# Kernel optimization log

Measured on AMD Instinct MI355X. Metric: run time of the kernel, lower is better.

The kernel has to match this reference:

```python
import jax, jax.numpy as jnp
import numpy as np

B, C, H, W = 8, 256, 48, 48
QC = C // 8                # query/key channels
MIP = max(8, C // 32)      # CoordAtt bottleneck channels
EPS = 1e-5                 # BatchNorm eps (inference, running_mean=0, running_var=1)


def _conv1x1(x, Wt, b=None):
    # 1x1 conv == channel matmul: x [b,c,h,w], Wt [o,c]
    y = jnp.einsum('bchw,oc->bohw', x, Wt)
    if b is not None:
        y = y + b[None, :, None, None]
    return y


def _bn(x, w, b):
    # inference BatchNorm with running_mean=0, running_var=1
    s = w * np.float32(1.0 / np.sqrt(1.0 + EPS))
    return x * s[None, :, None, None] + b[None, :, None, None]


def setup_inputs() -> dict:
    key = jax.random.key(0)
    ks = jax.random.split(key, 22)
    r = lambda k, sh, s=0.05: jax.random.normal(k, sh, jnp.float32) * s
    return dict(
        f1=jax.random.normal(ks[0], (B, C, H, W), jnp.float32),
        f2=jax.random.normal(ks[1], (B, C, H, W), jnp.float32),
        t1=r(ks[2], (1, C, 1, 1), 1.0),
        t2=r(ks[3], (1, C, 1, 1), 1.0),
        Wq=r(ks[4], (QC, C)), bq=r(ks[5], (QC,)),
        Wk=r(ks[6], (QC, C)), bk=r(ks[7], (QC,)),
        Wv=r(ks[8], (C, C)), bv=r(ks[9], (C,)),
        gamma=jnp.full((1,), 0.5, jnp.float32),
        ca_w1=r(ks[10], (MIP, C)), ca_b1=r(ks[11], (MIP,)),
        ca_bn_w=1.0 + r(ks[12], (MIP,)), ca_bn_b=r(ks[13], (MIP,)),
        ca_wh=r(ks[14], (C, MIP)), ca_bh=r(ks[15], (C,)),
        ca_ww=r(ks[16], (C, MIP)), ca_bw=r(ks[17], (C,)),
        fus_w=r(ks[18], (C, 2 * C)),
        fus_bn_w=1.0 + r(ks[19], (C,)), fus_bn_b=r(ks[20], (C,)),
    )


def _cross_attention(f1, f2, t1, t2, Wq, bq, Wk, bk, Wv, bv, gamma):
    b, c, h, w = f1.shape
    N = h * w
    f1e = f1 + t1
    f2e = f2 + t2

    def qkv(fe):
        q = _conv1x1(fe, Wq, bq).reshape(b, QC, N).transpose(0, 2, 1)  # [b,N,qc]
        k = _conv1x1(fe, Wk, bk).reshape(b, QC, N)                     # [b,qc,N]
        v = _conv1x1(fe, Wv, bv).reshape(b, c, N)                      # [b,c,N]
        return q, k, v

    q1, k1, v1 = qkv(f1e)
    q2, k2, v2 = qkv(f2e)

    # CrossAtt_1 = softmax(Q2 @ K1^T) applied to V1
    attn21 = jax.nn.softmax(jnp.einsum('bmq,bqn->bmn', q2, k1), axis=-1)  # [b,N,N]
    out1 = jnp.einsum('bcn,bmn->bcm', v1, attn21).reshape(b, c, h, w)
    # CrossAtt_2 = softmax(Q1 @ K2^T) applied to V2
    attn12 = jax.nn.softmax(jnp.einsum('bmq,bqn->bmn', q1, k2), axis=-1)
    out2 = jnp.einsum('bcn,bmn->bcm', v2, attn12).reshape(b, c, h, w)

    return gamma[0] * out1 + f1, gamma[0] * out2 + f2


def _coord_att(x, w1, b1, bnw, bnb, wh, bh, ww, bw):
    b, c, h, w = x.shape
    x_h = jnp.mean(x, axis=3, keepdims=True)                         # [b,c,h,1]
    x_w = jnp.mean(x, axis=2, keepdims=True).transpose(0, 1, 3, 2)   # [b,c,w,1]
    y = jnp.concatenate([x_h, x_w], axis=2)                          # [b,c,h+w,1]
    y = jax.nn.relu(_bn(_conv1x1(y, w1, b1), bnw, bnb))
    yh, yw = y[:, :, :h], y[:, :, h:]
    a_h = jax.nn.sigmoid(_conv1x1(yh, wh, bh))                       # [b,c,h,1]
    a_w = jax.nn.sigmoid(_conv1x1(yw.transpose(0, 1, 3, 2), ww, bw)) # [b,c,1,w]
    return x * a_w * a_h


def _fusion(x, Wf, bnw, bnb):
    return jax.nn.relu(_bn(_conv1x1(x, Wf), bnw, bnb))


def reference(f1, f2, t1, t2, Wq, bq, Wk, bk, Wv, bv, gamma,
              ca_w1, ca_b1, ca_bn_w, ca_bn_b, ca_wh, ca_bh, ca_ww, ca_bw,
              fus_w, fus_bn_w, fus_bn_b):
    a1, a2 = _cross_attention(f1, f2, t1, t2, Wq, bq, Wk, bk, Wv, bv, gamma)
    c1 = _coord_att(f1, ca_w1, ca_b1, ca_bn_w, ca_bn_b, ca_wh, ca_bh, ca_ww, ca_bw)
    c2 = _coord_att(f2, ca_w1, ca_b1, ca_bn_w, ca_bn_b, ca_wh, ca_bh, ca_ww, ca_bw)
    o1 = _fusion(jnp.concatenate([a1, c1], axis=1), fus_w, fus_bn_w, fus_bn_b)
    o2 = _fusion(jnp.concatenate([a2, c2], axis=1), fus_w, fus_bn_w, fus_bn_b)
    return o1, o2
```

## Files before the change

kernel.cpp:

```cpp
#include <hip/hip_runtime.h>
#include <hip/hip_bf16.h>

typedef unsigned short ushort_t;
typedef __attribute__((ext_vector_type(8))) short short8;
typedef __attribute__((ext_vector_type(4))) float floatx4;
typedef __attribute__((ext_vector_type(16))) float floatx16;
typedef __attribute__((ext_vector_type(4))) unsigned int uintx4;


__device__ __forceinline__ float bf2f(ushort_t u) {
    return __uint_as_float(((unsigned int)u) << 16);
}
__device__ __forceinline__ ushort_t f2bf(float f) {
    unsigned int x = __float_as_uint(f);
    unsigned int r = (x + 0x7fffu + ((x >> 16) & 1u)) >> 16;
    return (ushort_t)r;
}
__device__ __forceinline__ unsigned int pkbf(float a, float b) {
    __hip_bfloat162 h = __float22bfloat162_rn(float2{a, b});
    return *reinterpret_cast<unsigned int*>(&h);
}
__device__ __forceinline__ float loadIn(const void* p, size_t i, int isbf) {
    return isbf ? bf2f(((const ushort_t*)p)[i]) : ((const float*)p)[i];
}
__device__ __forceinline__ float fexp2(float x) {
#if __has_builtin(__builtin_amdgcn_exp2f)
    return __builtin_amdgcn_exp2f(x);
#else
    return exp2f(x);
#endif
}
__device__ __forceinline__ void plswap(unsigned& a, unsigned& b, int h) {
#if __has_builtin(__builtin_amdgcn_permlane32_swap)
    auto r = __builtin_amdgcn_permlane32_swap(a, b, false, false);
    a = r[0];
    b = r[1];
#else
    unsigned sa = __shfl_xor(a, 32), sb = __shfl_xor(b, 32);
    unsigned na = (h == 0) ? a : sb;
    unsigned nb = (h == 0) ? sa : b;
    a = na; b = nb;
#endif
}

#define BN_SCALE 0.9999950000374997f
#define LOG2E    1.4426950408889634f
#define ZERO16 (floatx16){0.f,0.f,0.f,0.f,0.f,0.f,0.f,0.f,0.f,0.f,0.f,0.f,0.f,0.f,0.f,0.f}

#define P_T1    0
#define P_T2    256
#define P_WQ    512
#define P_BQ    8704
#define P_WK    8768
#define P_BK    16960
#define P_WV    17024
#define P_BV    82560
#define P_GAMMA 82624
#define P_CAW1  82688
#define P_CAB1  84736
#define P_BNW   84800
#define P_BNB   84864
#define P_WH    84928
#define P_BH    86976
#define P_WW    87232
#define P_BW    89280
#define P_FUSW  89536
#define P_FBNW  220608
#define P_FBNB  220864
#define P_BQ2   221120

#define ATTN_BLOCKS 1152

__global__ void detect_kernel(const void* gamma, int* flag) {
    if (threadIdx.x == 0) {
        ushort_t u = ((const ushort_t*)gamma)[0];
        *flag = (u != 0) ? 1 : 0;
    }
}

__global__ __launch_bounds__(256) void convert_params(
    const void* t1, const void* t2, const void* Wq, const void* bq,
    const void* Wk, const void* bk, const void* Wv, const void* bv,
    const void* gm, const void* cw1, const void* cb1, const void* bnw,
    const void* bnb, const void* wh, const void* bh, const void* ww,
    const void* bw, const void* fw, const void* fbnw, const void* fbnb,
    const int* flagp, float* dst, ushort_t* WA, ushort_t* WF)
{
    int isbf = *flagp;
    const void* srcs[20] = {t1,t2,Wq,bq,Wk,bk,Wv,bv,gm,cw1,cb1,bnw,bnb,wh,bh,ww,bw,fw,fbnw,fbnb};
    const int   cnts[20] = {256,256,8192,32,8192,32,65536,256,1,2048,8,8,8,2048,256,2048,256,131072,256,256};
    const int   offs[20] = {P_T1,P_T2,P_WQ,P_BQ,P_WK,P_BK,P_WV,P_BV,P_GAMMA,P_CAW1,P_CAB1,
                            P_BNW,P_BNB,P_WH,P_BH,P_WW,P_BW,P_FUSW,P_FBNW,P_FBNB};
    int tid = blockIdx.x * 256 + threadIdx.x;
    int stride = gridDim.x * 256;
    #pragma unroll
    for (int sg = 0; sg < 20; sg++) {
        float* d = dst + offs[sg];
        for (int i = tid; i < cnts[sg]; i += stride) d[i] = loadIn(srcs[sg], i, isbf);
    }
    for (int i = tid; i < 81920; i += stride) {
        int o = i >> 8, c = i & 255;
        float v;
        if (o < 32)      v = loadIn(Wq, o * 256 + c, isbf);
        else if (o < 64) v = loadIn(Wk, (o - 32) * 256 + c, isbf);
        else             v = loadIn(Wv, (size_t)(o - 64) * 256 + c, isbf);
        WA[i] = f2bf(v);
    }
    for (int i = tid; i < 131072; i += stride) WF[i] = f2bf(loadIn(fw, i, isbf));
    int gw = tid >> 6, lane = tid & 63;
    if (gw < 640) {
        int side = gw / 320, o = gw % 320;
        const void* tsrc = side ? t2 : t1;
        float bias; const void* Wsrc; size_t wbase;
        if (o < 32)      { bias = loadIn(bq, o, isbf);       Wsrc = Wq; wbase = (size_t)o * 256; }
        else if (o < 64) { bias = loadIn(bk, o - 32, isbf);  Wsrc = Wk; wbase = (size_t)(o - 32) * 256; }
        else             { bias = loadIn(bv, o - 64, isbf);  Wsrc = Wv; wbase = (size_t)(o - 64) * 256; }
        float s = 0.f;
        for (int c = lane; c < 256; c += 64) s += loadIn(Wsrc, wbase + c, isbf) * loadIn(tsrc, c, isbf);
        s += __shfl_xor(s, 1);  s += __shfl_xor(s, 2);  s += __shfl_xor(s, 4);
        s += __shfl_xor(s, 8);  s += __shfl_xor(s, 16); s += __shfl_xor(s, 32);
        if (lane == 0) dst[P_BQ2 + gw] = bias + s;
    }
}

__global__ __launch_bounds__(256) void prep_qkv(
    const void* __restrict__ f1, const void* __restrict__ f2,
    const int* __restrict__ flagp,
    const ushort_t* __restrict__ WA, const float* __restrict__ P,
    ushort_t* __restrict__ fT,
    ushort_t* __restrict__ qG, ushort_t* __restrict__ kG, ushort_t* __restrict__ vG)
{
    __shared__ ushort_t xs[64][264];
    int isbf = *flagp;
    int blk = blockIdx.x;
    int nt = blk % 36, sb = blk / 36;
    int side = sb >> 3, b = sb & 7;
    int n0 = nt * 64;
    const void* f = side ? f2 : f1;
    int t = threadIdx.x;
    size_t base = ((size_t)b * 256 + t) * 2304 + n0;
    if (isbf) {
        const ushort_t* fp = (const ushort_t*)f + base;
        #pragma unroll
        for (int i = 0; i < 8; i++) {
            uint4 raw = *(const uint4*)&fp[i * 8];
            const ushort_t* rp = (const ushort_t*)&raw;
            #pragma unroll
            for (int j = 0; j < 8; j++) xs[i * 8 + j][t] = rp[j];
        }
    } else {
        const float* fp = (const float*)f + base;
        #pragma unroll
        for (int i = 0; i < 16; i++) {
            float4 raw = *(const float4*)&fp[i * 4];
            unsigned u0 = pkbf(raw.x, raw.y), u1 = pkbf(raw.z, raw.w);
            xs[i * 4 + 0][t] = (ushort_t)u0;
            xs[i * 4 + 1][t] = (ushort_t)(u0 >> 16);
            xs[i * 4 + 2][t] = (ushort_t)u1;
            xs[i * 4 + 3][t] = (ushort_t)(u1 >> 16);
        }
    }
    __syncthreads();
    #pragma unroll
    for (int i = 0; i < 8; i++) {
        int chunk = i * 256 + t;
        int row = chunk >> 5, k8 = (chunk & 31) * 8;
        *(uint4*)&fT[((size_t)sb * 2304 + n0 + row) * 256 + k8] = *(const uint4*)&xs[row][k8];
    }
    int w = t >> 6, l = t & 63, q = l >> 4, ln = l & 15;
    floatx4 acc[5][4];
    #pragma unroll
    for (int mi = 0; mi < 5; mi++)
        #pragma unroll
        for (int ns = 0; ns < 4; ns++) acc[mi][ns] = (floatx4){0.f, 0.f, 0.f, 0.f};
    #pragma unroll
    for (int ks = 0; ks < 8; ks++) {
        short8 a[5];
        #pragma unroll
        for (int mi = 0; mi < 5; mi++)
            a[mi] = *(const short8*)&WA[(size_t)(w * 80 + mi * 16 + ln) * 256 + ks * 32 + q * 8];
        #pragma unroll
        for (int ns = 0; ns < 4; ns++) {
            short8 bfr = *(const short8*)&xs[ns * 16 + ln][ks * 32 + q * 8];
            #pragma unroll
            for (int mi = 0; mi < 5; mi++)
                acc[mi][ns] = __builtin_amdgcn_mfma_f32_16x16x32_bf16(a[mi], bfr, acc[mi][ns], 0, 0, 0);
        }
    }
    const float* bp = P + P_BQ2 + side * 320;
    #pragma unroll
    for (int mi = 0; mi < 5; mi++) {
        int o0 = w * 80 + mi * 16 + q * 4;
        #pragma unroll
        for (int ns = 0; ns < 4; ns++) {
            int n = n0 + ns * 16 + ln;
            if (o0 < 32) {
                uint2 pk;
                pk.x = pkbf((acc[mi][ns][0] + bp[o0]) * LOG2E, (acc[mi][ns][1] + bp[o0 + 1]) * LOG2E);
                pk.y = pkbf((acc[mi][ns][2] + bp[o0 + 2]) * LOG2E, (acc[mi][ns][3] + bp[o0 + 3]) * LOG2E);
                *(uint2*)&qG[((size_t)sb * 2304 + n) * 32 + o0] = pk;
            } else if (o0 < 64) {
                uint2 pk;
                pk.x = pkbf(acc[mi][ns][0] + bp[o0], acc[mi][ns][1] + bp[o0 + 1]);
                pk.y = pkbf(acc[mi][ns][2] + bp[o0 + 2], acc[mi][ns][3] + bp[o0 + 3]);
                *(uint2*)&kG[((size_t)sb * 2304 + n) * 32 + (o0 - 32)] = pk;
            } else {
                unsigned u0 = pkbf(acc[mi][ns][0] + bp[o0], acc[mi][ns][1] + bp[o0 + 1]);
                unsigned u1 = pkbf(acc[mi][ns][2] + bp[o0 + 2], acc[mi][ns][3] + bp[o0 + 3]);
                vG[((size_t)sb * 256 + (o0 - 64 + 0)) * 2304 + n] = (ushort_t)u0;
                vG[((size_t)sb * 256 + (o0 - 64 + 1)) * 2304 + n] = (ushort_t)(u0 >> 16);
                vG[((size_t)sb * 256 + (o0 - 64 + 2)) * 2304 + n] = (ushort_t)u1;
                vG[((size_t)sb * 256 + (o0 - 64 + 3)) * 2304 + n] = (ushort_t)(u1 >> 16);
            }
        }
    }
}

__global__ __launch_bounds__(256) void pool_kernel(
    const ushort_t* __restrict__ fT, float* __restrict__ pools,
    float* __restrict__ lsum)
{
    int blk = blockIdx.x;
    int c = threadIdx.x;
    if (blk < 576 && c < 64) lsum[blk * 64 + c] = 0.f;
    int j = blk % 96, sb = blk / 96;
    const ushort_t* base = fT + (size_t)sb * 2304 * 256 + c;
    float s = 0.f;
    if (j < 48) {
        int h = j;
        #pragma unroll 8
        for (int w = 0; w < 48; w++) s += bf2f(base[(size_t)(h * 48 + w) * 256]);
    } else {
        int w = j - 48;
        #pragma unroll 8
        for (int h = 0; h < 48; h++) s += bf2f(base[(size_t)(h * 48 + w) * 256]);
    }
    pools[(size_t)sb * 24576 + c * 96 + j] = s * (1.f / 48.f);
}

__global__ __launch_bounds__(256) void attn_coord(
    const ushort_t* __restrict__ qG, const ushort_t* __restrict__ kG,
    const ushort_t* __restrict__ vG,
    ushort_t* __restrict__ O0, ushort_t* __restrict__ O1,
    float* __restrict__ lsum,
    const float* __restrict__ pools, const float* __restrict__ P,
    float* __restrict__ attv)
{
    __shared__ __align__(16) ushort_t vsm[4][64 * 68];
    __shared__ __align__(16) ushort_t paf[8192];

    int t = threadIdx.x;

    if (blockIdx.x >= ATTN_BLOCKS) {
        float* w1s = (float*)&vsm[0][0];
        float* ys  = w1s + 2048;
        int sb = blockIdx.x - ATTN_BLOCKS;
        for (int ff = t; ff < 2048; ff += 256) w1s[ff] = P[P_CAW1 + ff];
        __syncthreads();
        const float* pin = pools + (size_t)sb * 24576;
        if (t < 96) {
            float s[8];
            #pragma unroll
            for (int mp = 0; mp < 8; mp++) s[mp] = 0.f;
            for (int c = 0; c < 256; c++) {
                float p = pin[c * 96 + t];
                #pragma unroll
                for (int mp = 0; mp < 8; mp++) s[mp] += w1s[mp * 256 + c] * p;
            }
            #pragma unroll
            for (int mp = 0; mp < 8; mp++) {
                float vv = s[mp] + P[P_CAB1 + mp];
                vv = vv * (P[P_BNW + mp] * BN_SCALE) + P[P_BNB + mp];
                ys[mp * 96 + t] = fmaxf(vv, 0.f);
            }
        }
        __syncthreads();
        float* aout = attv + (size_t)sb * 24576;
        for (int ff = t; ff < 24576; ff += 256) {
            int j = ff >> 8, c = ff & 255;
            const float* W = P + ((j < 48) ? P_WH : P_WW);
            const float* B = P + ((j < 48) ? P_BH : P_BW);
            float s = B[c];
            #pragma unroll
            for (int mp = 0; mp < 8; mp++) s += W[c * 8 + mp] * ys[mp * 96 + j];
            aout[ff] = 1.f / (1.f + __expf(-s));
        }
        return;
    }

    int i = blockIdx.x;
    int xcd = i & 7, slot = i >> 3;
    int dhi = (slot >= 72) ? 1 : 0;
    int db = xcd + (dhi << 3);
    int rem = slot - 72 * dhi;
    int sp = rem & 1, mt = rem >> 1;
    int qsb = db ^ 8;

    int w = t >> 6;
    int qsw = w & 1, ksw = w >> 1;
    int l = t & 63, r31 = l & 31, h = l >> 5;
    int q0 = mt * 64, c0 = w * 64;

    short8 qf0, qf1;
    {
        const ushort_t* qrow = qG + ((size_t)qsb * 2304 + q0 + qsw * 32 + r31) * 32;
        qf0 = *(const short8*)&qrow[h * 8];
        qf1 = *(const short8*)&qrow[16 + h * 8];
    }

    const ushort_t* kW = kG + ((size_t)db * 2304 + ksw * 32 + r31) * 32 + h * 8;
    const ushort_t* vbase = vG + ((size_t)db * 256 + c0) * 2304;
    ushort_t* vw = &vsm[w][0];
    int vls = (l >> 3);
    int vlc = (l & 7) * 8;

    floatx16 o[2][2];
    #pragma unroll
    for (int qs = 0; qs < 2; qs++)
        #pragma unroll
        for (int cs = 0; cs < 2; cs++) o[qs][cs] = ZERO16;
    float l_lane = 0.f;

    int nstart = sp * 1152;

#define V_LOAD(VR, N0)                                                         \
    _Pragma("unroll")                                                          \
    for (int i_ = 0; i_ < 8; i_++) {                                           \
        int r_ = i_ * 8 + vls;                                                 \
        VR[i_] = *(const uint4*)&vbase[(size_t)r_ * 2304 + (N0) + vlc];        \
    }
#define V_STORE(VR)                                                            \
    _Pragma("unroll")                                                          \
    for (int i_ = 0; i_ < 8; i_++) {                                           \
        int a_ = (i_ * 8 + vls) * 68 + vlc;                                    \
        *(uint2*)&vw[a_]     = make_uint2(VR[i_].x, VR[i_].y);                 \
        *(uint2*)&vw[a_ + 4] = make_uint2(VR[i_].z, VR[i_].w);                 \
    }

#define DO_S_PUBLISH(K0, K1, BUF)                                              \
    {                                                                          \
        floatx16 s_ = ZERO16;                                                  \
        s_ = __builtin_amdgcn_mfma_f32_32x32x16_bf16(K0, qf0, s_, 0, 0, 0);    \
        s_ = __builtin_amdgcn_mfma_f32_32x32x16_bf16(K1, qf1, s_, 0, 0, 0);    \
        float e_[16];                                                          \
        _Pragma("unroll")                                                      \
        for (int r_ = 0; r_ < 16; r_++) e_[r_] = fexp2(s_[r_]);                \
        l_lane += (((e_[0] + e_[1]) + (e_[2] + e_[3]))                         \
                 + ((e_[4] + e_[5]) + (e_[6] + e_[7])))                        \
                + (((e_[8] + e_[9]) + (e_[10] + e_[11]))                       \
                 + ((e_[12] + e_[13]) + (e_[14] + e_[15])));                   \
        unsigned wd_[8];                                                       \
        _Pragma("unroll")                                                      \
        for (int p_ = 0; p_ < 8; p_++) wd_[p_] = pkbf(e_[2 * p_], e_[2 * p_ + 1]); \
        plswap(wd_[0], wd_[2], h); plswap(wd_[1], wd_[3], h);                  \
        plswap(wd_[4], wd_[6], h); plswap(wd_[5], wd_[7], h);                  \
        uintx4 A0_ = {wd_[0], wd_[1], wd_[2], wd_[3]};                         \
        uintx4 A1_ = {wd_[4], wd_[5], wd_[6], wd_[7]};                         \
        *(uintx4*)&paf[(size_t)((((BUF) * 2 + qsw) * 4 + ksw * 2 + 0) * 64 + l) * 8] = A0_; \
        *(uintx4*)&paf[(size_t)((((BUF) * 2 + qsw) * 4 + ksw * 2 + 1) * 64 + l) * 8] = A1_; \
    }

#define DO_PV(BUF)                                                             \
    __builtin_amdgcn_s_setprio(1);                                             \
    _Pragma("unroll")                                                          \
    for (int kt = 0; kt < 4; kt++) {                                           \
        short8 af0 = *(const short8*)&paf[(size_t)((((BUF) * 2 + 0) * 4 + kt) * 64 + l) * 8]; \
        short8 af1 = *(const short8*)&paf[(size_t)((((BUF) * 2 + 1) * 4 + kt) * 64 + l) * 8]; \
        _Pragma("unroll")                                                      \
        for (int cs = 0; cs < 2; cs++) {                                       \
            int va_ = (cs * 32 + r31) * 68 + kt * 16 + h * 8;                  \
            uint2 u0_ = *(const uint2*)&vw[va_];                               \
            uint2 u1_ = *(const uint2*)&vw[va_ + 4];                           \
            uintx4 vv_ = {u0_.x, u0_.y, u1_.x, u1_.y};                         \
            short8 vf_ = *(const short8*)&vv_;                                 \
            o[0][cs] = __builtin_amdgcn_mfma_f32_32x32x16_bf16(af0, vf_, o[0][cs], 0, 0, 0); \
            o[1][cs] = __builtin_amdgcn_mfma_f32_32x32x16_bf16(af1, vf_, o[1][cs], 0, 0, 0); \
        }                                                                      \
    }                                                                          \
    __builtin_amdgcn_s_setprio(0);

    uint4 vr[8];
    V_LOAD(vr, nstart)
    {
        const ushort_t* kp = kW + (size_t)nstart * 32;
        short8 k0 = *(const short8*)&kp[0];
        short8 k1 = *(const short8*)&kp[16];
        DO_S_PUBLISH(k0, k1, 0)
    }
    V_STORE(vr)
    __syncthreads();

    for (int tile = 0; tile < 17; tile++) {
        int n0 = nstart + tile * 64;
        int buf = tile & 1;
        const ushort_t* kp = kW + (size_t)(n0 + 64) * 32;
        short8 k0n = *(const short8*)&kp[0];
        short8 k1n = *(const short8*)&kp[16];
        V_LOAD(vr, n0 + 64)
        DO_PV(buf)
        DO_S_PUBLISH(k0n, k1n, (buf ^ 1))
        V_STORE(vr)
        __syncthreads();
    }
    DO_PV(1)
#undef DO_PV
#undef DO_S_PUBLISH
#undef V_STORE
#undef V_LOAD

    float lt = l_lane + __shfl_xor(l_lane, 32);
    if (h == 0)
        atomicAdd(&lsum[(size_t)db * 2304 + q0 + qsw * 32 + r31], lt);
    ushort_t* Op = sp ? O1 : O0;
    size_t obase = ((size_t)db * 2304 + q0) * 256 + c0;
    ushort_t* ow = vw;
    int rrow8 = l >> 3, rch0 = (l & 7) * 8;
    #pragma unroll
    for (int qs = 0; qs < 2; qs++) {
        #pragma unroll
        for (int cs = 0; cs < 2; cs++) {
            #pragma unroll
            for (int r = 0; r < 16; r++) {
                int qloc = (r & 3) + 8 * (r >> 2) + 4 * h;
                ow[qloc * 72 + cs * 32 + r31] = f2bf(o[qs][cs][r]);
            }
        }
        #pragma unroll
        for (int pass = 0; pass < 4; pass++) {
            int row = pass * 8 + rrow8;
            uintx4 v = *(const uintx4*)&ow[row * 72 + rch0];
            __builtin_nontemporal_store(v, (uintx4*)&Op[obase + (size_t)(qs * 32 + row) * 256 + rch0]);
        }
    }
}

__global__ __launch_bounds__(256) void fusion_gemm(
    const ushort_t* __restrict__ O0, const ushort_t* __restrict__ O1,
    const ushort_t* __restrict__ fT, const float* __restrict__ attv,
    const float* __restrict__ lsum,
    const ushort_t* __restrict__ WF, const float* __restrict__ P,
    const int* __restrict__ flagp, void* __restrict__ dout)
{
    __shared__ ushort_t xs[64][264];
    __shared__ float sS[64];
    int isbf = *flagp;
    int blk = blockIdx.x;
    int nt = blk % 36, sb = blk / 36;
    int n0 = nt * 64;
    int t = threadIdx.x;
    int w = t >> 6, l = t & 63, q = l >> 4, ln = l & 15;
    if (t < 64) {
        sS[t] = P[P_GAMMA] / lsum[(size_t)sb * 2304 + n0 + t];
    }
    __syncthreads();
    floatx4 acc[4][4];
    #pragma unroll
    for (int ms = 0; ms < 4; ms++)
        #pragma unroll
        for (int ns = 0; ns < 4; ns++) acc[ms][ns] = (floatx4){0.f, 0.f, 0.f, 0.f};
    size_t tbase = ((size_t)sb * 2304 + n0) * 256;
    #pragma unroll
    for (int i = 0; i < 8; i++) {
        int chunk = i * 256 + t;
        int row = chunk >> 5, k8 = (chunk & 31) * 8;
        size_t idx = tbase + (size_t)row * 256 + k8;
        uintx4 u0 = __builtin_nontemporal_load((const uintx4*)&O0[idx]);
        uintx4 u1 = __builtin_nontemporal_load((const uintx4*)&O1[idx]);
        uint4 uf = *(const uint4*)&fT[idx];
        const ushort_t* a0 = (const ushort_t*)&u0;
        const ushort_t* a1 = (const ushort_t*)&u1;
        const ushort_t* ff = (const ushort_t*)&uf;
        float s = sS[row];
        float v[8];
        #pragma unroll
        for (int j = 0; j < 8; j++) v[j] = (bf2f(a0[j]) + bf2f(a1[j])) * s + bf2f(ff[j]);
        uint4 pk;
        pk.x = pkbf(v[0], v[1]); pk.y = pkbf(v[2], v[3]);
        pk.z = pkbf(v[4], v[5]); pk.w = pkbf(v[6], v[7]);
        *(uint4*)&xs[row][k8] = pk;
    }
    __syncthreads();
    #pragma unroll
    for (int ks = 0; ks < 8; ks++) {
        short8 a[4];
        #pragma unroll
        for (int ms = 0; ms < 4; ms++)
            a[ms] = *(const short8*)&WF[(size_t)(w * 64 + ms * 16 + ln) * 512 + ks * 32 + q * 8];
        #pragma unroll
        for (int ns = 0; ns < 4; ns++) {
            short8 bfr = *(const short8*)&xs[ns * 16 + ln][ks * 32 + q * 8];
            #pragma unroll
            for (int ms = 0; ms < 4; ms++)
                acc[ms][ns] = __builtin_amdgcn_mfma_f32_16x16x32_bf16(a[ms], bfr, acc[ms][ns], 0, 0, 0);
        }
    }
    __syncthreads();
    const float* av = attv + (size_t)sb * 24576;
    #pragma unroll
    for (int i = 0; i < 8; i++) {
        int chunk = i * 256 + t;
        int row = chunk >> 5, k8 = (chunk & 31) * 8;
        int n = n0 + row;
        int h = n / 48, ww2 = n - h * 48;
        size_t idx = tbase + (size_t)row * 256 + k8;
        uint4 uf = *(const uint4*)&fT[idx];
        const ushort_t* ff = (const ushort_t*)&uf;
        float ah[8], aw[8];
        *(float4*)&ah[0] = *(const float4*)&av[h * 256 + k8];
        *(float4*)&ah[4] = *(const float4*)&av[h * 256 + k8 + 4];
        *(float4*)&aw[0] = *(const float4*)&av[(48 + ww2) * 256 + k8];
        *(float4*)&aw[4] = *(const float4*)&av[(48 + ww2) * 256 + k8 + 4];
        float v[8];
        #pragma unroll
        for (int j = 0; j < 8; j++) v[j] = bf2f(ff[j]) * ah[j] * aw[j];
        uint4 pk;
        pk.x = pkbf(v[0], v[1]); pk.y = pkbf(v[2], v[3]);
        pk.z = pkbf(v[4], v[5]); pk.w = pkbf(v[6], v[7]);
        *(uint4*)&xs[row][k8] = pk;
    }
    __syncthreads();
    #pragma unroll
    for (int ks = 0; ks < 8; ks++) {
        short8 a[4];
        #pragma unroll
        for (int ms = 0; ms < 4; ms++)
            a[ms] = *(const short8*)&WF[(size_t)(w * 64 + ms * 16 + ln) * 512 + 256 + ks * 32 + q * 8];
        #pragma unroll
        for (int ns = 0; ns < 4; ns++) {
            short8 bfr = *(const short8*)&xs[ns * 16 + ln][ks * 32 + q * 8];
            #pragma unroll
            for (int ms = 0; ms < 4; ms++)
                acc[ms][ns] = __builtin_amdgcn_mfma_f32_16x16x32_bf16(a[ms], bfr, acc[ms][ns], 0, 0, 0);
        }
    }
    #pragma unroll
    for (int ms = 0; ms < 4; ms++) {
        int o0 = w * 64 + ms * 16 + q * 4;
        float bw[4], bb[4];
        #pragma unroll
        for (int r = 0; r < 4; r++) {
            bw[r] = P[P_FBNW + o0 + r] * BN_SCALE;
            bb[r] = P[P_FBNB + o0 + r];
        }
        #pragma unroll
        for (int ns = 0; ns < 4; ns++) {
            int n = n0 + ns * 16 + ln;
            #pragma unroll
            for (int r = 0; r < 4; r++) {
                float v = acc[ms][ns][r] * bw[r] + bb[r];
                v = (v < 0.f) ? 0.f : v;
                size_t oidx = (size_t)sb * 589824 + (size_t)(o0 + r) * 2304 + n;
                if (isbf) ((ushort_t*)dout)[oidx] = f2bf(v);
                else      ((float*)dout)[oidx] = v;
            }
        }
    }
}

extern "C" void kernel_launch(void* const* d_in, const int* in_sizes, int n_in,
                              void* d_out, int out_size, void* d_ws, size_t ws_size,
                              hipStream_t stream) {
    const void* f1 = d_in[0]; const void* f2 = d_in[1];

    char* ws = (char*)d_ws;
    int*      flag  = (int*)(ws + 0);
    float*    P     = (float*)(ws + 1024);
    ushort_t* WA    = (ushort_t*)(ws + 917504);
    ushort_t* WF    = (ushort_t*)(ws + 1081344);
    ushort_t* fT    = (ushort_t*)(ws + 1343488);
    ushort_t* qG    = (ushort_t*)(ws + 20217856);
    ushort_t* kG    = (ushort_t*)(ws + 22577152);
    ushort_t* vG    = (ushort_t*)(ws + 24936448);
    ushort_t* O0    = (ushort_t*)(ws + 43810816);
    float*    pools = (float*)(ws + 62685184);
    float*    attv  = (float*)(ws + 64258048);
    ushort_t* O1    = (ushort_t*)(ws + 65830912);
    float*    lsum  = (float*)(ws + 917504);

    detect_kernel<<<dim3(1), dim3(64), 0, stream>>>(d_in[10], flag);
    convert_params<<<dim3(160), dim3(256), 0, stream>>>(
        d_in[2], d_in[3], d_in[4], d_in[5], d_in[6], d_in[7], d_in[8], d_in[9],
        d_in[10], d_in[11], d_in[12], d_in[13], d_in[14], d_in[15], d_in[16],
        d_in[17], d_in[18], d_in[19], d_in[20], d_in[21], flag, P, WA, WF);
    prep_qkv<<<dim3(576), dim3(256), 0, stream>>>(f1, f2, flag, WA, P, fT, qG, kG, vG);
    pool_kernel<<<dim3(1536), dim3(256), 0, stream>>>(fT, pools, lsum);
    attn_coord<<<dim3(1168), dim3(256), 0, stream>>>(qG, kG, vG, O0, O1, lsum, pools, P, attv);
    fusion_gemm<<<dim3(576), dim3(256), 0, stream>>>(
        O0, O1, fT, attv, lsum, WF, P, flag, d_out);
}
```

Measured before the change: 319.5 us.

## Stage V projection through shared memory for coalesced stores; launch coord blocks first

The V outputs of the QKV projection were written as scattered 2-byte stores along the channel-major layout. They are now staged in the shared tile in two 128-row halves and written back as 16-byte row-contiguous stores. Separately, the coordinate-attention blocks move to the start of the attention grid so they are scheduled early instead of trailing the attention blocks. The staging adds extra barriers and shared-memory traffic, and the shifted block indexing changes how attention blocks map to XCDs.

```diff
diff --git a/kernel.cpp b/kernel.cpp
--- a/kernel.cpp
+++ b/kernel.cpp
@@ -69,7 +69,7 @@
 #define P_FBNB  220864
 #define P_BQ2   221120
 
-#define ATTN_BLOCKS 1152
+#define COORD_BLOCKS 16
 
 __global__ void detect_kernel(const void* gamma, int* flag) {
     if (threadIdx.x == 0) {
@@ -191,6 +191,7 @@
     #pragma unroll
     for (int mi = 0; mi < 5; mi++) {
         int o0 = w * 80 + mi * 16 + q * 4;
+        if (o0 >= 64) continue;
         #pragma unroll
         for (int ns = 0; ns < 4; ns++) {
             int n = n0 + ns * 16 + ln;
@@ -199,19 +200,40 @@
                 pk.x = pkbf((acc[mi][ns][0] + bp[o0]) * LOG2E, (acc[mi][ns][1] + bp[o0 + 1]) * LOG2E);
                 pk.y = pkbf((acc[mi][ns][2] + bp[o0 + 2]) * LOG2E, (acc[mi][ns][3] + bp[o0 + 3]) * LOG2E);
                 *(uint2*)&qG[((size_t)sb * 2304 + n) * 32 + o0] = pk;
-            } else if (o0 < 64) {
+            } else {
                 uint2 pk;
                 pk.x = pkbf(acc[mi][ns][0] + bp[o0], acc[mi][ns][1] + bp[o0 + 1]);
                 pk.y = pkbf(acc[mi][ns][2] + bp[o0 + 2], acc[mi][ns][3] + bp[o0 + 3]);
                 *(uint2*)&kG[((size_t)sb * 2304 + n) * 32 + (o0 - 32)] = pk;
-            } else {
-                unsigned u0 = pkbf(acc[mi][ns][0] + bp[o0], acc[mi][ns][1] + bp[o0 + 1]);
-                unsigned u1 = pkbf(acc[mi][ns][2] + bp[o0 + 2], acc[mi][ns][3] + bp[o0 + 3]);
-                vG[((size_t)sb * 256 + (o0 - 64 + 0)) * 2304 + n] = (ushort_t)u0;
-                vG[((size_t)sb * 256 + (o0 - 64 + 1)) * 2304 + n] = (ushort_t)(u0 >> 16);
-                vG[((size_t)sb * 256 + (o0 - 64 + 2)) * 2304 + n] = (ushort_t)u1;
-                vG[((size_t)sb * 256 + (o0 - 64 + 3)) * 2304 + n] = (ushort_t)(u1 >> 16);
             }
+        }
+    }
+    ushort_t* vst = &xs[0][0];
+    ushort_t* vgb = vG + (size_t)sb * 256 * 2304;
+    int row8 = t >> 3, c8 = (t & 7) * 8;
+    #pragma unroll
+    for (int half = 0; half < 2; half++) {
+        __syncthreads();
+        int lo = 64 + half * 128;
+        #pragma unroll
+        for (int mi = 0; mi < 5; mi++) {
+            int o0 = w * 80 + mi * 16 + q * 4;
+            if (o0 < lo || o0 >= lo + 128) continue;
+            int vr0 = o0 - lo;
+            #pragma unroll
+            for (int ns = 0; ns < 4; ns++) {
+                int col = ns * 16 + ln;
+                #pragma unroll
+                for (int r = 0; r < 4; r++)
+                    vst[(vr0 + r) * 72 + col] = f2bf(acc[mi][ns][r] + bp[o0 + r]);
+            }
+        }
+        __syncthreads();
+        #pragma unroll
+        for (int pass = 0; pass < 4; pass++) {
+            int row = pass * 32 + row8;
+            uint4 v = *(const uint4*)&vst[row * 72 + c8];
+            *(uint4*)&vgb[(size_t)(half * 128 + row) * 2304 + n0 + c8] = v;
         }
     }
 }
@@ -251,10 +273,10 @@
 
     int t = threadIdx.x;
 
-    if (blockIdx.x >= ATTN_BLOCKS) {
+    if (blockIdx.x < COORD_BLOCKS) {
         float* w1s = (float*)&vsm[0][0];
         float* ys  = w1s + 2048;
-        int sb = blockIdx.x - ATTN_BLOCKS;
+        int sb = blockIdx.x;
         for (int ff = t; ff < 2048; ff += 256) w1s[ff] = P[P_CAW1 + ff];
         __syncthreads();
         const float* pin = pools + (size_t)sb * 24576;
@@ -288,7 +310,7 @@
         return;
     }
 
-    int i = blockIdx.x;
+    int i = blockIdx.x - COORD_BLOCKS;
     int xcd = i & 7, slot = i >> 3;
     int dhi = (slot >= 72) ? 1 : 0;
     int db = xcd + (dhi << 3);
```

Result: faster. 302.8 us (-5.2%).
